# Optimization experiments

Measured on AMD Instinct MI355X. Metric: run time of the kernel, lower is better.

## Reference

```python
import jax, jax.numpy as jnp
import numpy as np
import math


def _l2norm(x, axis):
    n = jnp.sqrt(jnp.sum(x * x, axis=axis, keepdims=True))
    return x / jnp.maximum(n, 1e-12)


def _look_back(x):
    # circular shift of buckets by one along dim1, concat along window dim2
    shift = jnp.concatenate([x[:, -1:], x[:, :-1]], axis=1)
    return jnp.concatenate([shift, x], axis=2)


def _get_dup_keys(x, rounds):
    # x: [B, L, K] int; counts duplicates of each key within its row
    idx = jnp.argsort(x, axis=-1)
    s = jnp.take_along_axis(x, idx, axis=-1)
    cnt = jnp.ones(x.shape, dtype=jnp.int32)
    for i in range(1, rounds):
        eq = (s[..., i:] == s[..., :-i]).astype(jnp.int32)
        cnt = cnt.at[..., i:].add(eq)
        cnt = cnt.at[..., :-i].add(eq)
    inv = jnp.argsort(idx, axis=-1)  # unsort
    return jnp.take_along_axis(cnt, inv, axis=-1)


def _forward(query, value, rand_matrix):
    B, L, dk = query.shape
    R = rand_matrix.shape[2]
    nb = 2 * rand_matrix.shape[3]          # n_buckets
    bl = L // nb                            # bucket_length

    # ---- LSH hashing ----
    rm = rand_matrix / jnp.linalg.norm(rand_matrix, axis=1, keepdims=True)
    q_n = _l2norm(query, -1)
    mm = jnp.einsum('bld,bdrn->blrn', q_n, rm)            # [B,L,R,nb/2]
    hashes = jnp.argmax(jnp.concatenate([mm, -mm], axis=-1), axis=-1).astype(jnp.int32)
    hashes = hashes * L + jnp.arange(L, dtype=jnp.int32)[None, :, None]  # [B,L,R]

    hash_indice = jnp.argsort(hashes, axis=1)             # sort positions per round
    sorted_hashes = jnp.take_along_axis(hashes, hash_indice, axis=1)
    original_indice = jnp.argsort(hash_indice, axis=1)    # inverse permutation

    def gather_bld(x, idx):  # x [B,L,dk], idx [B,L,R] -> [B,L,dk,R]
        xe = jnp.broadcast_to(x[..., None], (B, L, dk, R))
        ie = jnp.broadcast_to(idx[:, :, None, :], (B, L, dk, R))
        return jnp.take_along_axis(xe, ie, axis=1)

    rq = gather_bld(query, hash_indice).reshape(B, nb, bl, dk, R)
    lk = _l2norm(_look_back(rq), axis=-2)                 # [B,nb,2bl,dk,R]
    mqk = jnp.einsum('bnidr,bnjdr->bnijr', rq, lk) / math.sqrt(dk)  # [B,nb,bl,2bl,R]

    # bucket mismatch mask, then causal masks (order matters: == overwrites)
    sh = (sorted_hashes // L).reshape(B, nb, bl, R)
    mqk = jnp.where(sh[:, :, :, None, :] != _look_back(sh)[:, :, None, :, :], -1e9, mqk)
    qi = hash_indice.reshape(B, nb, bl, R).astype(jnp.int32)
    ki = _look_back(qi)                                    # [B,nb,2bl,R]
    mqk = jnp.where(qi[:, :, :, None, :] < ki[:, :, None, :, :], -1e9, mqk)
    mqk = jnp.where(qi[:, :, :, None, :] == ki[:, :, None, :, :], -1e5, mqk)

    # duplicate-key counts (computed in original order, regathered to sorted order)
    ki_full = jnp.broadcast_to(ki[:, :, None, :, :], (B, nb, bl, 2 * bl, R)).reshape(B, L, 2 * bl, R)
    oi = jnp.broadcast_to(original_indice[:, :, None, :], (B, L, 2 * bl, R))
    ki_orig = jnp.take_along_axis(ki_full, oi, axis=1)
    count_key = _get_dup_keys(ki_orig.reshape(B, L, 2 * bl * R), R).reshape(B, L, 2 * bl, R)
    hi = jnp.broadcast_to(hash_indice[:, :, None, :], (B, L, 2 * bl, R))
    count_key = jnp.take_along_axis(count_key, hi, axis=1)

    mqk_flat = mqk.reshape(B, L, 2 * bl, R)
    lse = jax.scipy.special.logsumexp(mqk_flat, axis=2)   # [B,L,R]
    sm = jnp.exp(mqk_flat - jnp.log(count_key.astype(mqk.dtype)) - lse[:, :, None, :])

    rv = gather_bld(value, hash_indice).reshape(B, nb, bl, dk, R)
    att = jnp.einsum('bnijr,bnjdr->bnidr', sm.reshape(B, nb, bl, 2 * bl, R), _look_back(rv))
    att = att.reshape(B, L, dk, R)
    di = jnp.broadcast_to(original_indice[:, :, None, :], (B, L, dk, R))
    att = jnp.take_along_axis(att, di, axis=1)             # back to original order

    lse_o = jnp.take_along_axis(lse, original_indice, axis=1)
    w = jax.nn.softmax(lse_o, axis=1)                      # faithful: dim=1 as in source
    return jnp.einsum('bldr,blr->bld', att, w)


def setup_inputs() -> dict:
    key = jax.random.key(0)
    k1, k2, k3 = jax.random.split(key, 3)
    B, L, DK, R, BL = 16, 4096, 64, 4, 64
    NB = L // BL
    query = jax.random.normal(k1, (B, L, DK), dtype=jnp.float32)
    value = jax.random.normal(k2, (B, L, DK), dtype=jnp.float32)
    rand_matrix = jax.random.normal(k3, (B, DK, R, NB // 2), dtype=jnp.float32)
    return {"query": query, "value": value, "rand_matrix": rand_matrix, "seed": 0}


def reference(query, value, rand_matrix, seed):
    # eval mode: deterministic_dropout is skipped; seed unused
    return _forward(query, value, rand_matrix)
```

## Files before the change

kernel.cpp:

```cpp
#include <hip/hip_runtime.h>

#define B_ 16
#define L_ 4096
#define DK_ 64
#define R_ 4
#define NB_ 64
#define BL_ 64

typedef __attribute__((ext_vector_type(8))) short bf16x8;
typedef __attribute__((ext_vector_type(4))) float f32x4;

__device__ __forceinline__ unsigned short f2bf(float f) {
  unsigned u = __float_as_uint(f);
  return (unsigned short)((u + 0x7FFFu + ((u >> 16) & 1u)) >> 16);
}
__device__ __forceinline__ float bf2f(unsigned short u) {
  return __uint_as_float(((unsigned)u) << 16);
}
__device__ __forceinline__ unsigned cvtpk(float lo, float hi) {
  unsigned r;
  asm("v_cvt_pk_bf16_f32 %0, %1, %2" : "=v"(r) : "v"(lo), "v"(hi));
  return r;
}
__device__ __forceinline__ int swz(int row) { return (row & 7) ^ ((row >> 3) & 7); }

__global__ __launch_bounds__(128) void prep_kernel(
    const float* __restrict__ rm, double* __restrict__ sinvd) {
  int b = blockIdx.x;
  int t = threadIdx.x;
  const float* rb = rm + (size_t)b * (DK_ * 128);
  double ss = 0.0;
  for (int d = 0; d < DK_; ++d) {
    double v = (double)rb[d * 128 + t];
    ss += v * v;
  }
  sinvd[b * 128 + t] = 1.0 / sqrt(ss);
}

__global__ __launch_bounds__(256) void hash_kernel(
    const float* __restrict__ query, const float* __restrict__ rm,
    const double* __restrict__ sinvd, int* __restrict__ bucket) {
  __shared__ float qs[64 * 68];
  __shared__ float rs[64 * 136];
  __shared__ double ssin[128];
  __shared__ int sb[64 * 4];

  int b = blockIdx.x >> 6;
  int tok0 = (blockIdx.x & 63) << 6;
  int t = threadIdx.x;

  {
    const float4* qg = (const float4*)(query + ((size_t)b * L_ + tok0) * DK_);
    #pragma unroll
    for (int u = 0; u < 4; ++u) {
      int i = t + u * 256;
      int tokl = i >> 4, c4 = i & 15;
      *(float4*)(qs + tokl * 68 + c4 * 4) = qg[i];
    }
  }
  {
    const float4* rg = (const float4*)(rm + (size_t)b * (DK_ * 128));
    #pragma unroll
    for (int u = 0; u < 8; ++u) {
      int i = t + u * 256;
      int d = i >> 5, c4 = i & 31;
      *(float4*)(rs + d * 136 + c4 * 4) = rg[i];
    }
  }
  if (t < 128) ssin[t] = sinvd[b * 128 + t];
  __syncthreads();

  int cg = t & 7;
  int tg = t >> 3;
  double acc0[16], acc1[16];
  #pragma unroll
  for (int j = 0; j < 16; ++j) { acc0[j] = 0.0; acc1[j] = 0.0; }

  const float* q0 = qs + (tg * 2 + 0) * 68;
  const float* q1 = qs + (tg * 2 + 1) * 68;
  const float* rp = rs + cg * 16;
  for (int d = 0; d < DK_; ++d) {
    double qa = (double)q0[d];
    double qb = (double)q1[d];
    const float* rr = rp + d * 136;
    #pragma unroll
    for (int j4 = 0; j4 < 4; ++j4) {
      float4 rv = *(const float4*)(rr + j4 * 4);
      double r0 = (double)rv.x, r1 = (double)rv.y,
             r2 = (double)rv.z, r3 = (double)rv.w;
      acc0[j4 * 4 + 0] += qa * r0; acc0[j4 * 4 + 1] += qa * r1;
      acc0[j4 * 4 + 2] += qa * r2; acc0[j4 * 4 + 3] += qa * r3;
      acc1[j4 * 4 + 0] += qb * r0; acc1[j4 * 4 + 1] += qb * r1;
      acc1[j4 * 4 + 2] += qb * r2; acc1[j4 * 4 + 3] += qb * r3;
    }
  }

  double bv0 = -1e300, bv1 = -1e300;
  int bi0 = 0, bi1 = 0;
  int nbase = (cg & 1) * 16;
  #pragma unroll
  for (int j = 0; j < 16; ++j) {
    int col = cg * 16 + j;
    double sv = ssin[col];
    int n = nbase + j;
    double v0 = acc0[j] * sv;
    double v1 = acc1[j] * sv;
    if (v0 > bv0 || (v0 == bv0 && n < bi0)) { bv0 = v0; bi0 = n; }
    if (-v0 > bv0 || (-v0 == bv0 && n + 32 < bi0)) { bv0 = -v0; bi0 = n + 32; }
    if (v1 > bv1 || (v1 == bv1 && n < bi1)) { bv1 = v1; bi1 = n; }
    if (-v1 > bv1 || (-v1 == bv1 && n + 32 < bi1)) { bv1 = -v1; bi1 = n + 32; }
  }
  {
    double ov = __shfl_xor(bv0, 1);
    int oi = __shfl_xor(bi0, 1);
    if (ov > bv0 || (ov == bv0 && oi < bi0)) { bv0 = ov; bi0 = oi; }
    ov = __shfl_xor(bv1, 1);
    oi = __shfl_xor(bi1, 1);
    if (ov > bv1 || (ov == bv1 && oi < bi1)) { bv1 = ov; bi1 = oi; }
  }
  if ((cg & 1) == 0) {
    int rr_ = cg >> 1;
    sb[(tg * 2 + 0) * 4 + rr_] = bi0;
    sb[(tg * 2 + 1) * 4 + rr_] = bi1;
  }
  __syncthreads();
  if (t < 64)
    ((int4*)bucket)[(size_t)b * L_ + tok0 + t] = ((int4*)sb)[t];
}

__global__ __launch_bounds__(1024) void sort_kernel(
    const int* __restrict__ bucket, int* __restrict__ sorted_pos,
    unsigned char* __restrict__ cpack) {
  int b = blockIdx.x >> 2;
  int r = blockIdx.x & 3;
  __shared__ int hist[64 * 65];
  __shared__ int off[64];
  int t = threadIdx.x, lane = t & 63, w = t >> 6;
  unsigned long long ltmask = (1ull << lane) - 1ull;
  const int* bb = bucket + (size_t)b * L_ * 4 + r;

  int binv[4], rank[4];
  #pragma unroll
  for (int u = 0; u < 4; ++u)
    binv[u] = bb[(size_t)((w * 4 + u) * 64 + lane) * 4];

  for (int idx = t; idx < 64 * 65; idx += 1024) hist[idx] = 0;
  __syncthreads();

  #pragma unroll
  for (int u = 0; u < 4; ++u) {
    int bin = binv[u];
    unsigned long long m = ~0ull;
    #pragma unroll
    for (int k = 0; k < 6; ++k) {
      unsigned long long bal = __ballot((bin >> k) & 1);
      m &= ((bin >> k) & 1) ? bal : ~bal;
    }
    rank[u] = (int)__popcll(m & ltmask);
    if (rank[u] == 0) hist[(w * 4 + u) * 65 + bin] = (int)__popcll(m);
  }
  __syncthreads();

  if (w == 0) {
    int run = 0;
    for (int g = 0; g < 64; ++g) {
      int v = hist[g * 65 + lane];
      hist[g * 65 + lane] = run;
      run += v;
    }
    int inc = run;
    #pragma unroll
    for (int d = 1; d < 64; d <<= 1) {
      int y = __shfl_up(inc, d, 64);
      if (lane >= d) inc += y;
    }
    off[lane] = inc - run;
  }
  __syncthreads();

  int* sp = sorted_pos + ((size_t)b * R_ + r) * L_;
  unsigned char* cp = cpack + (size_t)b * L_ * 4 + r;
  #pragma unroll
  for (int u = 0; u < 4; ++u) {
    int g = w * 4 + u;
    int bin = binv[u];
    int slot = off[bin] + hist[g * 65 + bin] + rank[u];
    sp[slot] = g * 64 + lane;
    cp[(size_t)(g * 64 + lane) * 4] = (unsigned char)(slot >> 6);
  }
}

__global__ __launch_bounds__(256) void attn_kernel(
    const float* __restrict__ query, const float* __restrict__ value,
    const int* __restrict__ sorted_pos, const int* __restrict__ bucket,
    const int* __restrict__ cpack,
    unsigned short* __restrict__ att, float* __restrict__ lse_s) {
  int wg = (int)blockIdx.x;
  wg = (wg & 7) * (B_ * R_ * NB_ / 8) + (wg >> 3);
  int n = wg & 63;
  int r = (wg >> 6) & 3;
  int b = wg >> 8;

  __shared__ __align__(16) short bufK[128 * 64];
  __shared__ __align__(16) short bufP[64 * 128];
  __shared__ float ssca[64];
  __shared__ int skpos[128];
  __shared__ int sbk[128];
  __shared__ int sckp[128];

  int t = threadIdx.x;
  const int* sp = sorted_pos + ((size_t)b * R_ + r) * L_;

  if (t < 128) {
    int chunk = (t < 64) ? ((n + 63) & 63) : n;
    int pos = sp[chunk * 64 + (t & 63)];
    skpos[t] = pos;
    sbk[t] = bucket[((size_t)b * L_ + pos) * 4 + r];
    sckp[t] = ((const int*)cpack)[(size_t)b * L_ + pos];
  }
  __syncthreads();

  {
    int j = t >> 1, half = t & 1;
    const float* qr = query + ((size_t)b * L_ + skpos[j]) * DK_ + half * 32;
    float v[32];
    float ss = 0.f;
    #pragma unroll
    for (int u = 0; u < 8; ++u) {
      float4 x = ((const float4*)qr)[u];
      v[u*4+0] = x.x; v[u*4+1] = x.y; v[u*4+2] = x.z; v[u*4+3] = x.w;
      ss += x.x*x.x + x.y*x.y + x.z*x.z + x.w*x.w;
    }
    ss += __shfl_xor(ss, 1);
    float inv = 1.0f / fmaxf(sqrtf(ss), 1e-12f);
    short* krow = bufK + j * 64;
    #pragma unroll
    for (int u = 0; u < 4; ++u) {
      int d0 = half * 32 + u * 8;
      uint4 pk;
      pk.x = cvtpk(v[u*8+0] * inv, v[u*8+1] * inv);
      pk.y = cvtpk(v[u*8+2] * inv, v[u*8+3] * inv);
      pk.z = cvtpk(v[u*8+4] * inv, v[u*8+5] * inv);
      pk.w = cvtpk(v[u*8+6] * inv, v[u*8+7] * inv);
      *(uint4*)(krow + (((d0 >> 3) ^ swz(j)) << 3)) = pk;
    }
    if (j >= 64 && half == 0) ssca[j - 64] = 0.125f / inv;
  }
  __syncthreads();

  int l = t & 63, w = t >> 6;
  f32x4 acc[8];
  #pragma unroll
  for (int tt = 0; tt < 8; ++tt) acc[tt] = (f32x4){0.f, 0.f, 0.f, 0.f};
  {
    int qrow = 64 + w * 16 + (l & 15);
    const short* qp_ = bufK + qrow * 64;
    bf16x8 a0 = *(const bf16x8*)(qp_ + ((((l >> 4)) ^ swz(qrow)) << 3));
    bf16x8 a1 = *(const bf16x8*)(qp_ + (((4 + (l >> 4)) ^ swz(qrow)) << 3));
    #pragma unroll
    for (int tt = 0; tt < 8; ++tt) {
      int krow = tt * 16 + (l & 15);
      const short* kp_ = bufK + krow * 64;
      bf16x8 b0 = *(const bf16x8*)(kp_ + ((((l >> 4)) ^ swz(krow)) << 3));
      bf16x8 b1 = *(const bf16x8*)(kp_ + (((4 + (l >> 4)) ^ swz(krow)) << 3));
      acc[tt] = __builtin_amdgcn_mfma_f32_16x16x32_bf16(a0, b0, acc[tt], 0, 0, 0);
      acc[tt] = __builtin_amdgcn_mfma_f32_16x16x32_bf16(a1, b1, acc[tt], 0, 0, 0);
    }
  }
  __syncthreads();

  int pi = t >> 2, qd = t & 3;
  const float* vr0 = value + ((size_t)b * L_ + skpos[2 * pi]) * DK_ + qd * 16;
  const float* vr1 = value + ((size_t)b * L_ + skpos[2 * pi + 1]) * DK_ + qd * 16;
  float4 va[4], vb4[4];
  #pragma unroll
  for (int c4 = 0; c4 < 4; ++c4) { va[c4] = ((const float4*)vr0)[c4]; vb4[c4] = ((const float4*)vr1)[c4]; }

  int kp[8], bk[8], ck[8];
  #pragma unroll
  for (int tt = 0; tt < 8; ++tt) {
    int col = tt * 16 + (l & 15);
    kp[tt] = skpos[col]; bk[tt] = sbk[col]; ck[tt] = sckp[col];
  }
  float st[8][4];
  float lse[4], psum[4];
  int qprow[4];
  #pragma unroll
  for (int j = 0; j < 4; ++j) {
    int qrow = w * 16 + (l >> 4) * 4 + j;
    int qp2 = skpos[64 + qrow];
    int bq = sbk[64 + qrow];
    float csc = ssca[qrow];
    qprow[j] = qp2;
    #pragma unroll
    for (int tt = 0; tt < 8; ++tt) {
      float s = acc[tt][j] * csc;
      s = ((qp2 < kp[tt]) || (bq != bk[tt])) ? -1e9f : s;
      s = (qp2 == kp[tt]) ? -1e5f : s;
      st[tt][j] = s;
    }
    float m = st[0][j];
    #pragma unroll
    for (int tt = 1; tt < 8; ++tt) m = fmaxf(m, st[tt][j]);
    m = fmaxf(m, __shfl_xor(m, 1));
    m = fmaxf(m, __shfl_xor(m, 2));
    m = fmaxf(m, __shfl_xor(m, 4));
    m = fmaxf(m, __shfl_xor(m, 8));
    float sum = 0.f;
    #pragma unroll
    for (int tt = 0; tt < 8; ++tt) { float e = __expf(st[tt][j] - m); st[tt][j] = e; sum += e; }
    sum += __shfl_xor(sum, 1);
    sum += __shfl_xor(sum, 2);
    sum += __shfl_xor(sum, 4);
    sum += __shfl_xor(sum, 8);
    psum[j] = sum;
    lse[j] = m + __logf(sum);
  }

  #pragma unroll
  for (int j = 0; j < 4; ++j) {
    int qrow = w * 16 + (l >> 4) * 4 + j;
    unsigned aq = (unsigned)sckp[64 + qrow] | 0x40404040u;
    float isum = 1.0f / psum[j];
    float pv[8];
    #pragma unroll
    for (int tt = 0; tt < 8; ++tt) {
      unsigned e = (aq - (unsigned)ck[tt]) & 0x3E3E3E3Eu;
      unsigned y = (e - 0x01010101u) & ~e & 0x80808080u;
      float cntf = (float)__popc(y);
      pv[tt] = st[tt][j] * isum * __builtin_amdgcn_rcpf(cntf);
    }
    short* prow = bufP + qrow * 128;
    int sz = swz(qrow);
    #pragma unroll
    for (int tp = 0; tp < 4; ++tp) {
      unsigned pr = cvtpk(pv[2 * tp], pv[2 * tp + 1]);
      int col0 = (2 * tp) * 16 + (l & 15);
      int col1 = col0 + 16;
      prow[(((col0 >> 3) ^ sz) << 3) + (col0 & 7)] = (short)pr;
      prow[(((col1 >> 3) ^ sz) << 3) + (col1 & 7)] = (short)(pr >> 16);
    }
  }
  if ((l & 15) == 0) {
    #pragma unroll
    for (int j = 0; j < 4; ++j)
      lse_s[((size_t)b * R_ + r) * L_ + qprow[j]] = lse[j];
  }

  short* VT = bufK;
  #pragma unroll
  for (int c4 = 0; c4 < 4; ++c4) {
    float4 x0 = va[c4], x1 = vb4[c4];
    #pragma unroll
    for (int cc = 0; cc < 4; ++cc) {
      float f0 = (cc == 0) ? x0.x : (cc == 1) ? x0.y : (cc == 2) ? x0.z : x0.w;
      float f1 = (cc == 0) ? x1.x : (cc == 1) ? x1.y : (cc == 2) ? x1.z : x1.w;
      unsigned pk2 = cvtpk(f0, f1);
      int nrow = qd * 16 + c4 * 4 + cc;
      int k0 = 2 * pi;
      int a = nrow * 128 + (((k0 >> 3) ^ swz(nrow)) << 3) + (k0 & 7);
      *(unsigned*)(VT + a) = pk2;
    }
  }
  __syncthreads();

  f32x4 o[4];
  #pragma unroll
  for (int nt = 0; nt < 4; ++nt) o[nt] = (f32x4){0.f, 0.f, 0.f, 0.f};
  {
    int qrow = w * 16 + (l & 15);
    #pragma unroll
    for (int ks = 0; ks < 4; ++ks) {
      bf16x8 pa = *(const bf16x8*)(bufP + qrow * 128 + (((ks * 4 + (l >> 4)) ^ swz(qrow)) << 3));
      #pragma unroll
      for (int nt = 0; nt < 4; ++nt) {
        int vrow = nt * 16 + (l & 15);
        bf16x8 vb = *(const bf16x8*)(VT + vrow * 128 + (((ks * 4 + (l >> 4)) ^ swz(vrow)) << 3));
        o[nt] = __builtin_amdgcn_mfma_f32_16x16x32_bf16(pa, vb, o[nt], 0, 0, 0);
      }
    }
  }

  #pragma unroll
  for (int jj = 0; jj < 4; ++jj) {
    unsigned short* arow = att + (((size_t)b * R_ + r) * L_ + qprow[jj]) * DK_;
    #pragma unroll
    for (int np = 0; np < 2; ++np) {
      unsigned pr = cvtpk(o[2 * np][jj], o[2 * np + 1][jj]);
      arow[(2 * np) * 16 + (l & 15)] = (unsigned short)pr;
      arow[(2 * np + 1) * 16 + (l & 15)] = (unsigned short)(pr >> 16);
    }
  }
}

__global__ __launch_bounds__(256) void lsered_kernel(
    const float* __restrict__ lse_s, float* __restrict__ wred) {
  int br = blockIdx.x;
  const float* row = lse_s + (size_t)br * L_;
  __shared__ float red[4];
  int t = threadIdx.x;
  float m = -1e30f;
  for (int p = t; p < L_; p += 256) m = fmaxf(m, row[p]);
  #pragma unroll
  for (int mask = 1; mask < 64; mask <<= 1) m = fmaxf(m, __shfl_xor(m, mask, 64));
  if ((t & 63) == 0) red[t >> 6] = m;
  __syncthreads();
  m = fmaxf(fmaxf(red[0], red[1]), fmaxf(red[2], red[3]));
  __syncthreads();
  float sum = 0.f;
  for (int p = t; p < L_; p += 256) sum += __expf(row[p] - m);
  #pragma unroll
  for (int mask = 1; mask < 64; mask <<= 1) sum += __shfl_xor(sum, mask, 64);
  if ((t & 63) == 0) red[t >> 6] = sum;
  __syncthreads();
  if (t == 0) {
    wred[br * 2] = m;
    wred[br * 2 + 1] = red[0] + red[1] + red[2] + red[3];
  }
}

__global__ __launch_bounds__(256) void combine_kernel(
    const unsigned short* __restrict__ att, const float* __restrict__ lse_s,
    const float* __restrict__ wred, float* __restrict__ out) {
  size_t idx = (size_t)blockIdx.x * 256 + threadIdx.x;
  int d4 = idx & 15;
  int l = (idx >> 4) & (L_ - 1);
  int b = (int)(idx >> 16);
  float4 o = make_float4(0.f, 0.f, 0.f, 0.f);
  #pragma unroll
  for (int r = 0; r < R_; ++r) {
    float m = wred[(b * R_ + r) * 2];
    float sinv = 1.0f / wred[(b * R_ + r) * 2 + 1];
    float w = __expf(lse_s[((size_t)b * R_ + r) * L_ + l] - m) * sinv;
    ushort4 a = *(const ushort4*)(att + ((((size_t)b * R_ + r) * L_ + l) * 16 + d4) * 4);
    o.x += w * bf2f(a.x); o.y += w * bf2f(a.y);
    o.z += w * bf2f(a.z); o.w += w * bf2f(a.w);
  }
  ((float4*)out)[idx] = o;
}

extern "C" void kernel_launch(void* const* d_in, const int* in_sizes, int n_in,
                              void* d_out, int out_size, void* d_ws, size_t ws_size,
                              hipStream_t stream) {
  const float* query = (const float*)d_in[0];
  const float* value = (const float*)d_in[1];
  const float* rm    = (const float*)d_in[2];
  (void)in_sizes; (void)n_in; (void)out_size; (void)ws_size;

  char* ws = (char*)d_ws;
  const size_t ATT_BYTES = (size_t)B_ * R_ * L_ * DK_ * 2;
  const size_t MB = 1048576;
  unsigned short* att        = (unsigned short*)ws;
  int*            bucket     = (int*)(ws + ATT_BYTES);
  int*            sorted_pos = (int*)(ws + ATT_BYTES + 1 * MB);
  unsigned char*  cpack      = (unsigned char*)(ws + ATT_BYTES + 2 * MB);
  float*          lse_s      = (float*)(ws + ATT_BYTES + 3 * MB);
  float*          wred       = (float*)(ws + ATT_BYTES + 4 * MB);
  double*         sinvd      = (double*)(ws + ATT_BYTES + 5 * MB);
  float* out = (float*)d_out;

  prep_kernel<<<B_, 128, 0, stream>>>(rm, sinvd);
  hash_kernel<<<B_ * 64, 256, 0, stream>>>(query, rm, sinvd, bucket);
  sort_kernel<<<B_ * R_, 1024, 0, stream>>>(bucket, sorted_pos, cpack);
  attn_kernel<<<B_ * R_ * NB_, 256, 0, stream>>>(query, value, sorted_pos, bucket,
                                                 (const int*)cpack, att, lse_s);
  lsered_kernel<<<B_ * R_, 256, 0, stream>>>(lse_s, wred);
  combine_kernel<<<(B_ * L_ * 16) / 256, 256, 0, stream>>>(att, lse_s, wred, out);
}
```

Measured before the change: 121.3 us.

## Transpose P·V MFMA operands, use exp2 softmax, widen combine per thread

The attention kernel now stores the probability tile transposed in a small per-wave padded LDS buffer. It swaps the MFMA operand order so each lane writes contiguous 4-element output runs with 8-byte stores, replacing scattered 2-byte global stores. The softmax scale is folded into log2e so exp2f/log2f can be used, with the lse converted back to natural log. The combine kernel handles four float4 outputs per thread and computes the per-round weights once. The P tile gather now uses scalar 16-bit LDS reads packed by hand, which may add LDS instructions.

```diff
diff --git a/kernel.cpp b/kernel.cpp
--- a/kernel.cpp
+++ b/kernel.cpp
@@ -10,10 +10,6 @@
 typedef __attribute__((ext_vector_type(8))) short bf16x8;
 typedef __attribute__((ext_vector_type(4))) float f32x4;
 
-__device__ __forceinline__ unsigned short f2bf(float f) {
-  unsigned u = __float_as_uint(f);
-  return (unsigned short)((u + 0x7FFFu + ((u >> 16) & 1u)) >> 16);
-}
 __device__ __forceinline__ float bf2f(unsigned short u) {
   return __uint_as_float(((unsigned)u) << 16);
 }
@@ -202,7 +198,7 @@
   int b = wg >> 8;
 
   __shared__ __align__(16) short bufK[128 * 64];
-  __shared__ __align__(16) short bufP[64 * 128];
+  __shared__ __align__(16) unsigned short ptb[4 * 2560];
   __shared__ float ssca[64];
   __shared__ int skpos[128];
   __shared__ int sbk[128];
@@ -244,7 +240,7 @@
       pk.w = cvtpk(v[u*8+6] * inv, v[u*8+7] * inv);
       *(uint4*)(krow + (((d0 >> 3) ^ swz(j)) << 3)) = pk;
     }
-    if (j >= 64 && half == 0) ssca[j - 64] = 0.125f / inv;
+    if (j >= 64 && half == 0) ssca[j - 64] = 0.18033688f / inv;
   }
   __syncthreads();
 
@@ -296,7 +292,7 @@
     for (int tt = 0; tt < 8; ++tt) {
       float s = acc[tt][j] * csc;
       s = ((qp2 < kp[tt]) || (bq != bk[tt])) ? -1e9f : s;
-      s = (qp2 == kp[tt]) ? -1e5f : s;
+      s = (qp2 == kp[tt]) ? -144269.5f : s;
       st[tt][j] = s;
     }
     float m = st[0][j];
@@ -308,13 +304,13 @@
     m = fmaxf(m, __shfl_xor(m, 8));
     float sum = 0.f;
     #pragma unroll
-    for (int tt = 0; tt < 8; ++tt) { float e = __expf(st[tt][j] - m); st[tt][j] = e; sum += e; }
+    for (int tt = 0; tt < 8; ++tt) { float e = exp2f(st[tt][j] - m); st[tt][j] = e; sum += e; }
     sum += __shfl_xor(sum, 1);
     sum += __shfl_xor(sum, 2);
     sum += __shfl_xor(sum, 4);
     sum += __shfl_xor(sum, 8);
     psum[j] = sum;
-    lse[j] = m + __logf(sum);
+    lse[j] = 0.69314718f * (m + __log2f(sum));
   }
 
   #pragma unroll
@@ -322,29 +318,30 @@
     int qrow = w * 16 + (l >> 4) * 4 + j;
     unsigned aq = (unsigned)sckp[64 + qrow] | 0x40404040u;
     float isum = 1.0f / psum[j];
-    float pv[8];
     #pragma unroll
     for (int tt = 0; tt < 8; ++tt) {
       unsigned e = (aq - (unsigned)ck[tt]) & 0x3E3E3E3Eu;
       unsigned y = (e - 0x01010101u) & ~e & 0x80808080u;
       float cntf = (float)__popc(y);
-      pv[tt] = st[tt][j] * isum * __builtin_amdgcn_rcpf(cntf);
-    }
-    short* prow = bufP + qrow * 128;
-    int sz = swz(qrow);
-    #pragma unroll
-    for (int tp = 0; tp < 4; ++tp) {
-      unsigned pr = cvtpk(pv[2 * tp], pv[2 * tp + 1]);
-      int col0 = (2 * tp) * 16 + (l & 15);
-      int col1 = col0 + 16;
-      prow[(((col0 >> 3) ^ sz) << 3) + (col0 & 7)] = (short)pr;
-      prow[(((col1 >> 3) ^ sz) << 3) + (col1 & 7)] = (short)(pr >> 16);
+      st[tt][j] = st[tt][j] * isum * __builtin_amdgcn_rcpf(cntf);
     }
   }
   if ((l & 15) == 0) {
     #pragma unroll
     for (int j = 0; j < 4; ++j)
       lse_s[((size_t)b * R_ + r) * L_ + qprow[j]] = lse[j];
+  }
+
+  {
+    unsigned short* PT = ptb + w * 2560;
+    int q0 = (l >> 4) * 4;
+    #pragma unroll
+    for (int tt = 0; tt < 8; ++tt) {
+      unsigned u0 = cvtpk(st[tt][0], st[tt][1]);
+      unsigned u1 = cvtpk(st[tt][2], st[tt][3]);
+      int krow = tt * 16 + (l & 15);
+      *(uint2*)(PT + krow * 20 + q0) = make_uint2(u0, u1);
+    }
   }
 
   short* VT = bufK;
@@ -368,27 +365,32 @@
   #pragma unroll
   for (int nt = 0; nt < 4; ++nt) o[nt] = (f32x4){0.f, 0.f, 0.f, 0.f};
   {
-    int qrow = w * 16 + (l & 15);
+    const unsigned short* PTr = ptb + w * 2560;
     #pragma unroll
     for (int ks = 0; ks < 4; ++ks) {
-      bf16x8 pa = *(const bf16x8*)(bufP + qrow * 128 + (((ks * 4 + (l >> 4)) ^ swz(qrow)) << 3));
+      int basePT = (ks * 32 + (l >> 4) * 8) * 20 + (l & 15);
+      union { uint4 u; bf16x8 v; } bp;
+      bp.u.x = (unsigned)PTr[basePT]       | ((unsigned)PTr[basePT + 20] << 16);
+      bp.u.y = (unsigned)PTr[basePT + 40]  | ((unsigned)PTr[basePT + 60] << 16);
+      bp.u.z = (unsigned)PTr[basePT + 80]  | ((unsigned)PTr[basePT + 100] << 16);
+      bp.u.w = (unsigned)PTr[basePT + 120] | ((unsigned)PTr[basePT + 140] << 16);
       #pragma unroll
       for (int nt = 0; nt < 4; ++nt) {
         int vrow = nt * 16 + (l & 15);
-        bf16x8 vb = *(const bf16x8*)(VT + vrow * 128 + (((ks * 4 + (l >> 4)) ^ swz(vrow)) << 3));
-        o[nt] = __builtin_amdgcn_mfma_f32_16x16x32_bf16(pa, vb, o[nt], 0, 0, 0);
+        bf16x8 av = *(const bf16x8*)(VT + vrow * 128 + (((ks * 4 + (l >> 4)) ^ swz(vrow)) << 3));
+        o[nt] = __builtin_amdgcn_mfma_f32_16x16x32_bf16(av, bp.v, o[nt], 0, 0, 0);
       }
     }
   }
 
-  #pragma unroll
-  for (int jj = 0; jj < 4; ++jj) {
-    unsigned short* arow = att + (((size_t)b * R_ + r) * L_ + qprow[jj]) * DK_;
-    #pragma unroll
-    for (int np = 0; np < 2; ++np) {
-      unsigned pr = cvtpk(o[2 * np][jj], o[2 * np + 1][jj]);
-      arow[(2 * np) * 16 + (l & 15)] = (unsigned short)pr;
-      arow[(2 * np + 1) * 16 + (l & 15)] = (unsigned short)(pr >> 16);
+  {
+    int qpos = skpos[64 + w * 16 + (l & 15)];
+    unsigned short* arow = att + (((size_t)b * R_ + r) * L_ + qpos) * DK_;
+    #pragma unroll
+    for (int nt = 0; nt < 4; ++nt) {
+      unsigned p0 = cvtpk(o[nt][0], o[nt][1]);
+      unsigned p1 = cvtpk(o[nt][2], o[nt][3]);
+      *(uint2*)(arow + nt * 16 + (l >> 4) * 4) = make_uint2(p0, p1);
     }
   }
 }
@@ -422,21 +424,29 @@
 __global__ __launch_bounds__(256) void combine_kernel(
     const unsigned short* __restrict__ att, const float* __restrict__ lse_s,
     const float* __restrict__ wred, float* __restrict__ out) {
-  size_t idx = (size_t)blockIdx.x * 256 + threadIdx.x;
-  int d4 = idx & 15;
-  int l = (idx >> 4) & (L_ - 1);
-  int b = (int)(idx >> 16);
-  float4 o = make_float4(0.f, 0.f, 0.f, 0.f);
+  int idx = blockIdx.x * 256 + threadIdx.x;
+  int dq = idx & 3;
+  int l = (idx >> 2) & (L_ - 1);
+  int b = idx >> 14;
+  float wv[4];
   #pragma unroll
   for (int r = 0; r < R_; ++r) {
     float m = wred[(b * R_ + r) * 2];
     float sinv = 1.0f / wred[(b * R_ + r) * 2 + 1];
-    float w = __expf(lse_s[((size_t)b * R_ + r) * L_ + l] - m) * sinv;
-    ushort4 a = *(const ushort4*)(att + ((((size_t)b * R_ + r) * L_ + l) * 16 + d4) * 4);
-    o.x += w * bf2f(a.x); o.y += w * bf2f(a.y);
-    o.z += w * bf2f(a.z); o.w += w * bf2f(a.w);
-  }
-  ((float4*)out)[idx] = o;
+    wv[r] = __expf(lse_s[((size_t)b * R_ + r) * L_ + l] - m) * sinv;
+  }
+  #pragma unroll
+  for (int u = 0; u < 4; ++u) {
+    int d4 = dq * 4 + u;
+    float4 o = make_float4(0.f, 0.f, 0.f, 0.f);
+    #pragma unroll
+    for (int r = 0; r < R_; ++r) {
+      ushort4 a = *(const ushort4*)(att + ((((size_t)b * R_ + r) * L_ + l) * 16 + d4) * 4);
+      o.x += wv[r] * bf2f(a.x); o.y += wv[r] * bf2f(a.y);
+      o.z += wv[r] * bf2f(a.z); o.w += wv[r] * bf2f(a.w);
+    }
+    ((float4*)out)[((size_t)b * L_ + l) * 16 + d4] = o;
+  }
 }
 
 extern "C" void kernel_launch(void* const* d_in, const int* in_sizes, int n_in,
@@ -465,5 +475,5 @@
   attn_kernel<<<B_ * R_ * NB_, 256, 0, stream>>>(query, value, sorted_pos, bucket,
                                                  (const int*)cpack, att, lse_s);
   lsered_kernel<<<B_ * R_, 256, 0, stream>>>(lse_s, wred);
-  combine_kernel<<<(B_ * L_ * 16) / 256, 256, 0, stream>>>(att, lse_s, wred, out);
-}
+  combine_kernel<<<(B_ * L_ * 4) / 256, 256, 0, stream>>>(att, lse_s, wred, out);
+}
```

Measured after the change: 122.8 us. Within noise of the previous version (+1.2%).
